# Kernel tuning notes

Measured on AMD Instinct MI355X. Metric: run time of the kernel, lower is better.

## Reference

```python
import jax, jax.numpy as jnp
import numpy as np

N, E, D_IN, D_AGG, D_OUT = 40000, 640000, 128, 128, 64


def setup_inputs() -> dict:
    key = jax.random.key(0)
    ks = jax.random.split(key, 16)

    def lin(kw, fan_in, fan_out):
        s = 1.0 / np.sqrt(fan_in)
        return jax.random.uniform(kw, (fan_in, fan_out), jnp.float32, -s, s)

    return {
        "x_self": jax.random.normal(ks[0], (N, D_IN), jnp.float32),
        "x_neighbor": jax.random.normal(ks[1], (N, D_AGG), jnp.float32),
        "edge_index": jax.random.randint(ks[2], (2, E), 0, N, jnp.int64),
        # linear_in_self: D_IN -> 2*D_OUT
        "W_in_self": lin(ks[3], D_IN, 2 * D_OUT),
        "b_in_self": jnp.zeros((2 * D_OUT,), jnp.float32),
        # linear_out_self: D_IN + 2*D_OUT -> D_OUT
        "W_out_self": lin(ks[4], D_IN + 2 * D_OUT, D_OUT),
        "b_out_self": jnp.zeros((D_OUT,), jnp.float32),
        # gcn1: D_IN -> 2*D_OUT ; gcn2: 2*D_OUT -> D_OUT
        "Wg1": lin(ks[5], D_IN, 2 * D_OUT),
        "bg1": jnp.zeros((2 * D_OUT,), jnp.float32),
        "Wg2": lin(ks[6], 2 * D_OUT, D_OUT),
        "bg2": jnp.zeros((D_OUT,), jnp.float32),
        # linear_out: D_AGG + D_OUT -> D_OUT
        "W_out": lin(ks[7], D_AGG + D_OUT, D_OUT),
        "b_out": jnp.zeros((D_OUT,), jnp.float32),
    }


def _gcn(x, W, b, row, col, norm, n):
    # PyG GCNConv: linear transform, then normalized gather/scatter-add
    h = x @ W                              # [N, out]
    msg = h[row] * norm[:, None]           # [E+N, out] gathered messages
    return jax.ops.segment_sum(msg, col, num_segments=n) + b


def reference(x_self, x_neighbor, edge_index,
              W_in_self, b_in_self, W_out_self, b_out_self,
              Wg1, bg1, Wg2, bg2, W_out, b_out):
    n = x_self.shape[0]
    loop = jnp.arange(n, dtype=edge_index.dtype)
    row = jnp.concatenate([edge_index[0], loop])   # sources (+ self-loops)
    col = jnp.concatenate([edge_index[1], loop])   # targets (+ self-loops)
    deg = jax.ops.segment_sum(jnp.ones_like(col, jnp.float32), col, num_segments=n)
    dis = jnp.where(deg > 0, jax.lax.rsqrt(jnp.maximum(deg, 1.0)), 0.0)
    norm = dis[row] * dis[col]

    # self branch
    l1 = jax.nn.relu(x_self @ W_in_self + b_in_self)
    l1 = jnp.concatenate([x_self, l1], axis=1)
    l1 = l1 @ W_out_self + b_out_self

    # GCN aggregation branch (no activation between convs, per source)
    g1 = _gcn(x_self, Wg1, bg1, row, col, norm, n)
    g2 = _gcn(g1, Wg2, bg2, row, col, norm, n)
    x2 = jnp.concatenate([x_neighbor, g2], axis=1) @ W_out + b_out
    return (l1, x2)
```

## Files before the change

kernel.cpp:

```cpp
#include <hip/hip_runtime.h>

typedef short s8v __attribute__((ext_vector_type(8)));
typedef float f4v __attribute__((ext_vector_type(4)));
typedef unsigned short u16x8 __attribute__((ext_vector_type(8)));

__device__ __forceinline__ unsigned short f2bf(float f) {
  unsigned u = __float_as_uint(f);
  u = (u + 0x7fffu + ((u >> 16) & 1u)) >> 16;
  return (unsigned short)u;
}
__device__ __forceinline__ float bf2f(unsigned short s) {
  return __uint_as_float(((unsigned)s) << 16);
}

#define SLOTS 64

__device__ __forceinline__ void pack_one(const float* __restrict__ W,
                                         unsigned short* __restrict__ P,
                                         int NCf, int stride, int t) {
  const int lane = t & 63;
  const int ct = (t >> 6) % (NCf / 16);
  const int kc = (t >> 6) / (NCf / 16);
  const int col = ct * 16 + (lane & 15);
  const int krow = kc * 32 + (lane >> 4) * 8;
  unsigned short tmp[8];
#pragma unroll
  for (int j = 0; j < 8; ++j) tmp[j] = f2bf(W[(krow + j) * stride + col]);
  uint4 o;
  o.x = (unsigned)tmp[0] | ((unsigned)tmp[1] << 16);
  o.y = (unsigned)tmp[2] | ((unsigned)tmp[3] << 16);
  o.z = (unsigned)tmp[4] | ((unsigned)tmp[5] << 16);
  o.w = (unsigned)tmp[6] | ((unsigned)tmp[7] << 16);
  reinterpret_cast<uint4*>(P)[t] = o;
}

__global__ __launch_bounds__(256) void prep_kernel(
    const float* __restrict__ x, unsigned short* __restrict__ S1,
    int* __restrict__ cnt, const float* __restrict__ Wis,
    const float* __restrict__ Wos, const float* __restrict__ Wo,
    unsigned short* __restrict__ P, int cvtB, int zeroB, int N) {
  const int blk = blockIdx.x;
  const int tid = threadIdx.x;
  if (blk < cvtB) {
    const int i = blk * 256 + tid;
    const float4 v = reinterpret_cast<const float4*>(x)[i];
    ushort4 o;
    o.x = f2bf(v.x); o.y = f2bf(v.y); o.z = f2bf(v.z); o.w = f2bf(v.w);
    reinterpret_cast<ushort4*>(S1)[i] = o;
    return;
  }
  const int b1 = blk - cvtB;
  if (b1 < zeroB) {
    const int i = b1 * 256 + tid;
    if (i < N) cnt[i] = 0;
    return;
  }
  const int b = b1 - zeroB;
  if (b < 4)        pack_one(Wis,            P + 0,     64, 128, b * 256 + tid);
  else if (b < 8)   pack_one(Wis + 64,       P + 8192,  64, 128, (b - 4) * 256 + tid);
  else if (b < 12)  pack_one(Wos,            P + 16384, 64, 64,  (b - 8) * 256 + tid);
  else if (b < 16)  pack_one(Wos + 128 * 64, P + 24576, 64, 64,  (b - 12) * 256 + tid);
  else if (b < 20)  pack_one(Wo,             P + 32768, 64, 64,  (b - 16) * 256 + tid);
  else              pack_one(Wo + 128 * 64,  P + 40960, 64, 64,  (b - 20) * 256 + tid);
}

__device__ __forceinline__ void stage16k(unsigned short* __restrict__ Bs,
                                         const unsigned short* __restrict__ src) {
  uint4* d = reinterpret_cast<uint4*>(Bs);
  const uint4* s = reinterpret_cast<const uint4*>(src);
  for (int i = threadIdx.x; i < 1024; i += 256) d[i] = s[i];
}

__device__ __forceinline__ void load_a_bf16(s8v a[4],
                                            const unsigned short* __restrict__ A,
                                            int arow, int koff) {
#pragma unroll
  for (int kc = 0; kc < 4; ++kc)
    a[kc] = *reinterpret_cast<const s8v*>(A + (long long)arow * 128 + kc * 32 + koff);
}

__device__ __forceinline__ void mfma_panel(f4v acc[4], const s8v a[4],
                                           const unsigned short* __restrict__ Bs,
                                           int lane) {
#pragma unroll
  for (int kc = 0; kc < 4; ++kc)
#pragma unroll
    for (int ct = 0; ct < 4; ++ct) {
      const s8v b =
          *reinterpret_cast<const s8v*>(&Bs[((kc * 4 + ct) * 64 + lane) * 8]);
      acc[ct] = __builtin_amdgcn_mfma_f32_16x16x32_bf16(a[kc], b, acc[ct], 0, 0, 0);
    }
}

__device__ __forceinline__ void gemm1_body(
    unsigned short* __restrict__ Bs, const unsigned short* __restrict__ S1,
    const unsigned short* __restrict__ P, const float* __restrict__ bis,
    unsigned short* __restrict__ S2h, int blk) {
  const int tid = threadIdx.x;
  const int wave = tid >> 6, lane = tid & 63;
  const int row0 = blk * 64 + wave * 16;
  const int arow = row0 + (lane & 15);
  const int koff = (lane >> 4) * 8;
  s8v a1[4];
  load_a_bf16(a1, S1, arow, koff);
  f4v acc[8] = {};
#pragma unroll
  for (int h = 0; h < 2; ++h) {
    if (h) __syncthreads();
    stage16k(Bs, P + h * 8192);
    __syncthreads();
    mfma_panel(&acc[h * 4], a1, Bs, lane);
  }
  const int crow0 = row0 + (lane >> 4) * 4;
  const int ccol = lane & 15;
#pragma unroll
  for (int h = 0; h < 2; ++h)
#pragma unroll
    for (int ctl = 0; ctl < 4; ++ctl) {
      const int col = h * 64 + ctl * 16 + ccol;
      const float bv = bis[col];
#pragma unroll
      for (int r = 0; r < 4; ++r) {
        const float v = fmaxf(acc[h * 4 + ctl][r] + bv, 0.f);
        S2h[(long long)(crow0 + r) * 128 + col] = f2bf(v);
      }
    }
}

__device__ __forceinline__ void gemm2_body(
    unsigned short* __restrict__ Bs, const unsigned short* __restrict__ S1,
    const unsigned short* __restrict__ S2h, const unsigned short* __restrict__ P0,
    const unsigned short* __restrict__ P1, const float* __restrict__ bos,
    float* __restrict__ out1, int blk) {
  const int tid = threadIdx.x;
  const int wave = tid >> 6, lane = tid & 63;
  const int row0 = blk * 64 + wave * 16;
  const int arow = row0 + (lane & 15);
  const int koff = (lane >> 4) * 8;
  s8v a1[4], a2[4];
  load_a_bf16(a1, S1, arow, koff);
  load_a_bf16(a2, S2h, arow, koff);
  f4v acc[4] = {};
  stage16k(Bs, P0);
  __syncthreads();
  mfma_panel(acc, a1, Bs, lane);
  __syncthreads();
  stage16k(Bs, P1);
  __syncthreads();
  mfma_panel(acc, a2, Bs, lane);
  const int crow0 = row0 + (lane >> 4) * 4;
  const int ccol = lane & 15;
#pragma unroll
  for (int ct = 0; ct < 4; ++ct) {
    const int col = ct * 16 + ccol;
    const float bv = bos[col];
#pragma unroll
    for (int r = 0; r < 4; ++r)
      out1[(long long)(crow0 + r) * 64 + col] = acc[ct][r] + bv;
  }
}

template <int K1, bool OUT_BF16, bool A1F32, bool ACCUM>
__device__ __forceinline__ void gemm64_body(
    unsigned short* __restrict__ Bs, const void* __restrict__ A1v,
    const unsigned short* __restrict__ P1, const float* __restrict__ bias,
    void* __restrict__ Cout, int blk) {
  constexpr int KC1 = K1 / 32;
  const int tid = threadIdx.x;
  {
    uint4* d = reinterpret_cast<uint4*>(Bs);
    const uint4* s = reinterpret_cast<const uint4*>(P1);
    constexpr int n1 = K1 * 64 / 8;
    for (int i = tid; i < n1; i += 256) d[i] = s[i];
  }
  const int wave = tid >> 6, lane = tid & 63;
  const int row0 = blk * 64 + wave * 16;
  const int arow = row0 + (lane & 15);
  const int koff = (lane >> 4) * 8;
  s8v a1[KC1];
  if constexpr (A1F32) {
    const float* A1f = (const float*)A1v;
#pragma unroll
    for (int kc = 0; kc < KC1; ++kc) {
      const float4 f0 = *reinterpret_cast<const float4*>(
          A1f + (long long)arow * K1 + kc * 32 + koff);
      const float4 f1 = *reinterpret_cast<const float4*>(
          A1f + (long long)arow * K1 + kc * 32 + koff + 4);
      s8v r;
      r[0] = (short)f2bf(f0.x); r[1] = (short)f2bf(f0.y);
      r[2] = (short)f2bf(f0.z); r[3] = (short)f2bf(f0.w);
      r[4] = (short)f2bf(f1.x); r[5] = (short)f2bf(f1.y);
      r[6] = (short)f2bf(f1.z); r[7] = (short)f2bf(f1.w);
      a1[kc] = r;
    }
  } else {
    const unsigned short* A1b = (const unsigned short*)A1v;
#pragma unroll
    for (int kc = 0; kc < KC1; ++kc)
      a1[kc] = *reinterpret_cast<const s8v*>(A1b + (long long)arow * K1 +
                                             kc * 32 + koff);
  }
  __syncthreads();
  f4v acc[4] = {};
#pragma unroll
  for (int kc = 0; kc < KC1; ++kc)
#pragma unroll
    for (int ct = 0; ct < 4; ++ct) {
      const s8v b =
          *reinterpret_cast<const s8v*>(&Bs[((kc * 4 + ct) * 64 + lane) * 8]);
      acc[ct] = __builtin_amdgcn_mfma_f32_16x16x32_bf16(a1[kc], b, acc[ct], 0, 0, 0);
    }
  const int crow0 = row0 + (lane >> 4) * 4;
  const int ccol = lane & 15;
#pragma unroll
  for (int ct = 0; ct < 4; ++ct) {
    const int col = ct * 16 + ccol;
    const float bv = bias ? bias[col] : 0.f;
#pragma unroll
    for (int r = 0; r < 4; ++r) {
      const long long idx = (long long)(crow0 + r) * 64 + col;
      float v = acc[ct][r] + bv;
      if (ACCUM) v += ((float*)Cout)[idx];
      if (OUT_BF16)
        ((unsigned short*)Cout)[idx] = f2bf(v);
      else
        ((float*)Cout)[idx] = v;
    }
  }
}

template <bool PASS_B>
__device__ __forceinline__ void gather_body(
    const unsigned short* __restrict__ h, const int* __restrict__ csrS,
    const int* __restrict__ cnt, const float* __restrict__ dis,
    float* __restrict__ s_out, const float* __restrict__ s_in,
    const float* __restrict__ bvec, const float* __restrict__ bias,
    unsigned short* __restrict__ out, int N, int gb, int nblk) {
  const int wid = (gb * 256 + (int)threadIdx.x) >> 6;
  const int lane = threadIdx.x & 63;
  const int grp = lane >> 3;
  const int sl = lane & 7;
  const int stride = nblk * 32;

  float bb[8], bv[8];
  if constexpr (PASS_B) {
    const float4 b0 = *reinterpret_cast<const float4*>(bias + sl * 8);
    const float4 b1 = *reinterpret_cast<const float4*>(bias + sl * 8 + 4);
    bb[0] = b0.x; bb[1] = b0.y; bb[2] = b0.z; bb[3] = b0.w;
    bb[4] = b1.x; bb[5] = b1.y; bb[6] = b1.z; bb[7] = b1.w;
    const float4 v0 = *reinterpret_cast<const float4*>(bvec + sl * 8);
    const float4 v1 = *reinterpret_cast<const float4*>(bvec + sl * 8 + 4);
    bv[0] = v0.x; bv[1] = v0.y; bv[2] = v0.z; bv[3] = v0.w;
    bv[4] = v1.x; bv[5] = v1.y; bv[6] = v1.z; bv[7] = v1.w;
  }

  for (int n = wid * 8 + grp; n < N; n += stride) {
    const float dn = dis[n];
    const float dn2 = dn * dn;
    float a[8];
    {
      const u16x8 hv =
          *reinterpret_cast<const u16x8*>(h + (long long)n * 64 + sl * 8);
#pragma unroll
      for (int q = 0; q < 8; ++q) a[q] = bf2f(hv[q]) * dn2;
    }
    float sw = dn2;
    const int deg = min(cnt[n], SLOTS);
    const int* base = csrS + (long long)n * SLOTS;
    int j = 0;
    for (; j + 3 < deg; j += 4) {
      const int4 e = *reinterpret_cast<const int4*>(base + j);
      const u16x8 u0 =
          *reinterpret_cast<const u16x8*>(h + (long long)e.x * 64 + sl * 8);
      const u16x8 u1 =
          *reinterpret_cast<const u16x8*>(h + (long long)e.y * 64 + sl * 8);
      const u16x8 u2 =
          *reinterpret_cast<const u16x8*>(h + (long long)e.z * 64 + sl * 8);
      const u16x8 u3 =
          *reinterpret_cast<const u16x8*>(h + (long long)e.w * 64 + sl * 8);
      const float w0 = dis[e.x] * dn, w1 = dis[e.y] * dn;
      const float w2 = dis[e.z] * dn, w3 = dis[e.w] * dn;
#pragma unroll
      for (int q = 0; q < 8; ++q) {
        a[q] = fmaf(bf2f(u0[q]), w0, a[q]);
        a[q] = fmaf(bf2f(u1[q]), w1, a[q]);
        a[q] = fmaf(bf2f(u2[q]), w2, a[q]);
        a[q] = fmaf(bf2f(u3[q]), w3, a[q]);
      }
      if constexpr (!PASS_B) sw += (w0 + w1) + (w2 + w3);
    }
    for (; j < deg; ++j) {
      const int r = base[j];
      const u16x8 u =
          *reinterpret_cast<const u16x8*>(h + (long long)r * 64 + sl * 8);
      const float w = dis[r] * dn;
#pragma unroll
      for (int q = 0; q < 8; ++q) a[q] = fmaf(bf2f(u[q]), w, a[q]);
      if constexpr (!PASS_B) sw += w;
    }
    u16x8 o;
    if constexpr (!PASS_B) {
      if (sl == 0) s_out[n] = sw;
#pragma unroll
      for (int q = 0; q < 8; ++q) o[q] = f2bf(a[q]);
    } else {
      const float si = s_in[n];
#pragma unroll
      for (int q = 0; q < 8; ++q) o[q] = f2bf(fmaf(si, bv[q], a[q] + bb[q]));
    }
    *reinterpret_cast<u16x8*>(out + (long long)n * 64 + sl * 8) = o;
  }
}

__global__ __launch_bounds__(256) void mega_kernel(
    const unsigned short* __restrict__ S1, const float* __restrict__ x_nb,
    const unsigned short* __restrict__ P, unsigned short* __restrict__ P12,
    const float* __restrict__ bis, const float* __restrict__ bo,
    const float* __restrict__ Wg1, const float* __restrict__ Wg2,
    const float* __restrict__ bg1, float* __restrict__ bvec,
    unsigned short* __restrict__ S2h, unsigned short* __restrict__ S4,
    float* __restrict__ out2, const int* __restrict__ rows,
    const int* __restrict__ cols, int* __restrict__ cnt,
    int* __restrict__ csrS, int E, int degB, int GB) {
  __shared__ unsigned short Bs[8192];
  const int b = blockIdx.x;
  if (b < degB) {
    const int i = b * 256 + (int)threadIdx.x;
    if (i < E) {
      const int c = cols[i];
      const int pos = atomicAdd(&cnt[c], 1);
      if (pos < SLOTS) csrS[(long long)c * SLOTS + pos] = rows[i];
    }
  } else if (b < degB + 33) {
    const int w = b - degB;
    if (w < 32) {
      const int t = w * 256 + (int)threadIdx.x;
      const int i = t >> 6, j = t & 63;
      float acc = 0.f;
      for (int k = 0; k < 128; ++k)
        acc = fmaf(Wg1[i * 128 + k], Wg2[k * 64 + j], acc);
      const int kc = i >> 5;
      const int lane = ((i >> 3) & 3) * 16 + (j & 15);
      const int jj = i & 7;
      const int ct = j >> 4;
      P12[((kc * 4 + ct) * 64 + lane) * 8 + jj] = f2bf(acc);
    } else if (threadIdx.x < 64) {
      const int j = threadIdx.x;
      float acc = 0.f;
      for (int k = 0; k < 128; ++k) acc = fmaf(bg1[k], Wg2[k * 64 + j], acc);
      bvec[j] = acc;
    }
  } else if (b < degB + 33 + GB) {
    gemm64_body<128, false, true, false>(Bs, x_nb, P + 32768, bo, out2,
                                         b - degB - 33);
  } else if (b < degB + 33 + 2 * GB) {
    gemm1_body(Bs, S1, P, bis, S2h, b - degB - 33 - GB);
  } else {
    gemm64_body<128, true, false, false>(Bs, S1, P + 45056, nullptr, S4,
                                         b - degB - 33 - 2 * GB);
  }
}

__global__ __launch_bounds__(256) void dis_kernel(const int* __restrict__ cnt,
                                                  float* __restrict__ dis,
                                                  int N) {
  const int i = blockIdx.x * 256 + threadIdx.x;
  if (i < N) dis[i] = rsqrtf((float)cnt[i] + 1.0f);
}

__global__ __launch_bounds__(256) void g2ga_kernel(
    const unsigned short* __restrict__ S1, const unsigned short* __restrict__ S2h,
    const unsigned short* __restrict__ P, const float* __restrict__ bos,
    float* __restrict__ out1, const unsigned short* __restrict__ S4,
    const int* __restrict__ csrS, const int* __restrict__ cnt,
    const float* __restrict__ dis, float* __restrict__ s_out,
    unsigned short* __restrict__ S3, int N, int GB, int GGB) {
  __shared__ unsigned short Bs[8192];
  const int b = blockIdx.x;
  if (b < GGB) {
    gather_body<false>(S4, csrS, cnt, dis, s_out, nullptr, nullptr, nullptr,
                       S3, N, b, GGB);
  } else {
    gemm2_body(Bs, S1, S2h, P + 16384, P + 24576, bos, out1, b - GGB);
  }
}

__global__ __launch_bounds__(256) void gatherB_kernel(
    const unsigned short* __restrict__ S3, const int* __restrict__ csrS,
    const int* __restrict__ cnt, const float* __restrict__ dis,
    const float* __restrict__ s_in, const float* __restrict__ bvec,
    const float* __restrict__ bias, unsigned short* __restrict__ G2, int N) {
  gather_body<true>(S3, csrS, cnt, dis, nullptr, s_in, bvec, bias, G2, N,
                    blockIdx.x, gridDim.x);
}

__global__ __launch_bounds__(256) void g4b_kernel(
    const unsigned short* __restrict__ G2, const unsigned short* __restrict__ P,
    float* __restrict__ out2) {
  __shared__ unsigned short Bs[4096];
  gemm64_body<64, false, false, true>(Bs, G2, P + 40960, nullptr, out2,
                                      blockIdx.x);
}

extern "C" void kernel_launch(void* const* d_in, const int* in_sizes, int n_in,
                              void* d_out, int out_size, void* d_ws,
                              size_t ws_size, hipStream_t stream) {
  const float* x_self = (const float*)d_in[0];
  const float* x_nb = (const float*)d_in[1];
  const int* ei = (const int*)d_in[2];
  const float* Wis = (const float*)d_in[3];
  const float* bis = (const float*)d_in[4];
  const float* Wos = (const float*)d_in[5];
  const float* bos = (const float*)d_in[6];
  const float* Wg1 = (const float*)d_in[7];
  const float* bg1 = (const float*)d_in[8];
  const float* Wg2 = (const float*)d_in[9];
  const float* bg2 = (const float*)d_in[10];
  const float* Wo = (const float*)d_in[11];
  const float* bo = (const float*)d_in[12];

  const int N = in_sizes[0] / 128;
  const int E = (int)(in_sizes[2] / 2);
  const int* rows = ei;
  const int* cols = ei + E;

  float* out1 = (float*)d_out;
  float* out2 = out1 + (long long)N * 64;

  float* dis = (float*)d_ws;
  int* cnt = (int*)(dis + N);
  float* s = (float*)(cnt + N);
  float* bvec = s + N;
  int* csrS = (int*)(bvec + 64);
  unsigned short* S1 = (unsigned short*)(csrS + (long long)N * SLOTS);
  unsigned short* S2h = S1 + (long long)N * 128;
  unsigned short* S3 = S2h + (long long)N * 128;
  unsigned short* S4 = S3 + (long long)N * 64;
  unsigned short* P = S4 + (long long)N * 64;
  unsigned short* pW12 = P + 45056;

  const int GB = N / 64;
  const int GGB = (N + 31) / 32;

  const int cvtB = (N * 32 + 255) / 256;
  const int zeroB = (N + 255) / 256;
  const int degB = (E + 255) / 256;

  prep_kernel<<<cvtB + zeroB + 22, 256, 0, stream>>>(
      x_self, S1, cnt, Wis, Wos, Wo, P, cvtB, zeroB, N);
  mega_kernel<<<degB + 33 + 3 * GB, 256, 0, stream>>>(
      S1, x_nb, P, pW12, bis, bo, Wg1, Wg2, bg1, bvec, S2h, S4, out2, rows,
      cols, cnt, csrS, E, degB, GB);
  dis_kernel<<<zeroB, 256, 0, stream>>>(cnt, dis, N);
  g2ga_kernel<<<GGB + GB, 256, 0, stream>>>(S1, S2h, P, bos, out1, S4, csrS,
                                            cnt, dis, s, S3, N, GB, GGB);
  gatherB_kernel<<<GGB, 256, 0, stream>>>(S3, csrS, cnt, dis, s, bvec, bg2, S1, N);
  g4b_kernel<<<GB, 256, 0, stream>>>(S1, P, out2);
}
```

Baseline: 115.1 us.

## Drop bf16 pre-conversion and dis kernel; fuse conversion into GEMM loads

Removes the separate fp32-to-bf16 conversion of x_self and has the GEMMs load fp32 directly and convert in registers. The dis kernel is eliminated by recomputing rsqrt(cnt+1) inline in the gathers. The Wg1*Wg2 product and the bias fold move into the prep kernel, and the CSR fill now reads four edges per thread. This cuts one launch and a write/read pass over a bf16 copy of x_self. In exchange the fp32 GEMM loads are twice as wide, the gathers do an extra rsqrt per neighbour, and E is assumed divisible by 4.

After: 105.0 us. 1.1x faster.

```diff
diff --git a/kernel.cpp b/kernel.cpp
--- a/kernel.cpp
+++ b/kernel.cpp
@@ -34,34 +34,42 @@
   reinterpret_cast<uint4*>(P)[t] = o;
 }
 
-__global__ __launch_bounds__(256) void prep_kernel(
-    const float* __restrict__ x, unsigned short* __restrict__ S1,
+__global__ __launch_bounds__(256) void prepA_kernel(
     int* __restrict__ cnt, const float* __restrict__ Wis,
     const float* __restrict__ Wos, const float* __restrict__ Wo,
-    unsigned short* __restrict__ P, int cvtB, int zeroB, int N) {
+    const float* __restrict__ Wg1, const float* __restrict__ Wg2,
+    const float* __restrict__ bg1, unsigned short* __restrict__ P,
+    float* __restrict__ bvec, int zeroB, int N) {
   const int blk = blockIdx.x;
   const int tid = threadIdx.x;
-  if (blk < cvtB) {
+  if (blk < zeroB) {
     const int i = blk * 256 + tid;
-    const float4 v = reinterpret_cast<const float4*>(x)[i];
-    ushort4 o;
-    o.x = f2bf(v.x); o.y = f2bf(v.y); o.z = f2bf(v.z); o.w = f2bf(v.w);
-    reinterpret_cast<ushort4*>(S1)[i] = o;
-    return;
-  }
-  const int b1 = blk - cvtB;
-  if (b1 < zeroB) {
-    const int i = b1 * 256 + tid;
     if (i < N) cnt[i] = 0;
     return;
   }
-  const int b = b1 - zeroB;
+  const int b = blk - zeroB;
   if (b < 4)        pack_one(Wis,            P + 0,     64, 128, b * 256 + tid);
   else if (b < 8)   pack_one(Wis + 64,       P + 8192,  64, 128, (b - 4) * 256 + tid);
   else if (b < 12)  pack_one(Wos,            P + 16384, 64, 64,  (b - 8) * 256 + tid);
   else if (b < 16)  pack_one(Wos + 128 * 64, P + 24576, 64, 64,  (b - 12) * 256 + tid);
   else if (b < 20)  pack_one(Wo,             P + 32768, 64, 64,  (b - 16) * 256 + tid);
-  else              pack_one(Wo + 128 * 64,  P + 40960, 64, 64,  (b - 20) * 256 + tid);
+  else if (b < 22)  pack_one(Wo + 128 * 64,  P + 40960, 64, 64,  (b - 20) * 256 + tid);
+  else if (b < 54) {
+    const int t = (b - 22) * 256 + tid;
+    const int i = t >> 6, j = t & 63;
+    float acc = 0.f;
+    for (int k = 0; k < 128; ++k)
+      acc = fmaf(Wg1[i * 128 + k], Wg2[k * 64 + j], acc);
+    const int kc = i >> 5;
+    const int lane = ((i >> 3) & 3) * 16 + (j & 15);
+    const int jj = i & 7;
+    const int ct = j >> 4;
+    (P + 45056)[((kc * 4 + ct) * 64 + lane) * 8 + jj] = f2bf(acc);
+  } else if (tid < 64) {
+    float acc = 0.f;
+    for (int k = 0; k < 128; ++k) acc = fmaf(bg1[k], Wg2[k * 64 + tid], acc);
+    bvec[tid] = acc;
+  }
 }
 
 __device__ __forceinline__ void stage16k(unsigned short* __restrict__ Bs,
@@ -79,6 +87,24 @@
     a[kc] = *reinterpret_cast<const s8v*>(A + (long long)arow * 128 + kc * 32 + koff);
 }
 
+__device__ __forceinline__ void load_a_f32(s8v a[4],
+                                           const float* __restrict__ A,
+                                           int arow, int koff) {
+#pragma unroll
+  for (int kc = 0; kc < 4; ++kc) {
+    const float4 f0 = *reinterpret_cast<const float4*>(
+        A + (long long)arow * 128 + kc * 32 + koff);
+    const float4 f1 = *reinterpret_cast<const float4*>(
+        A + (long long)arow * 128 + kc * 32 + koff + 4);
+    s8v r;
+    r[0] = (short)f2bf(f0.x); r[1] = (short)f2bf(f0.y);
+    r[2] = (short)f2bf(f0.z); r[3] = (short)f2bf(f0.w);
+    r[4] = (short)f2bf(f1.x); r[5] = (short)f2bf(f1.y);
+    r[6] = (short)f2bf(f1.z); r[7] = (short)f2bf(f1.w);
+    a[kc] = r;
+  }
+}
+
 __device__ __forceinline__ void mfma_panel(f4v acc[4], const s8v a[4],
                                            const unsigned short* __restrict__ Bs,
                                            int lane) {
@@ -93,7 +119,7 @@
 }
 
 __device__ __forceinline__ void gemm1_body(
-    unsigned short* __restrict__ Bs, const unsigned short* __restrict__ S1,
+    unsigned short* __restrict__ Bs, const float* __restrict__ x,
     const unsigned short* __restrict__ P, const float* __restrict__ bis,
     unsigned short* __restrict__ S2h, int blk) {
   const int tid = threadIdx.x;
@@ -102,7 +128,7 @@
   const int arow = row0 + (lane & 15);
   const int koff = (lane >> 4) * 8;
   s8v a1[4];
-  load_a_bf16(a1, S1, arow, koff);
+  load_a_f32(a1, x, arow, koff);
   f4v acc[8] = {};
 #pragma unroll
   for (int h = 0; h < 2; ++h) {
@@ -128,7 +154,7 @@
 }
 
 __device__ __forceinline__ void gemm2_body(
-    unsigned short* __restrict__ Bs, const unsigned short* __restrict__ S1,
+    unsigned short* __restrict__ Bs, const float* __restrict__ x,
     const unsigned short* __restrict__ S2h, const unsigned short* __restrict__ P0,
     const unsigned short* __restrict__ P1, const float* __restrict__ bos,
     float* __restrict__ out1, int blk) {
@@ -138,7 +164,7 @@
   const int arow = row0 + (lane & 15);
   const int koff = (lane >> 4) * 8;
   s8v a1[4], a2[4];
-  load_a_bf16(a1, S1, arow, koff);
+  load_a_f32(a1, x, arow, koff);
   load_a_bf16(a2, S2h, arow, koff);
   f4v acc[4] = {};
   stage16k(Bs, P0);
@@ -232,10 +258,10 @@
 template <bool PASS_B>
 __device__ __forceinline__ void gather_body(
     const unsigned short* __restrict__ h, const int* __restrict__ csrS,
-    const int* __restrict__ cnt, const float* __restrict__ dis,
-    float* __restrict__ s_out, const float* __restrict__ s_in,
-    const float* __restrict__ bvec, const float* __restrict__ bias,
-    unsigned short* __restrict__ out, int N, int gb, int nblk) {
+    const int* __restrict__ cnt, float* __restrict__ s_out,
+    const float* __restrict__ s_in, const float* __restrict__ bvec,
+    const float* __restrict__ bias, unsigned short* __restrict__ out, int N,
+    int gb, int nblk) {
   const int wid = (gb * 256 + (int)threadIdx.x) >> 6;
   const int lane = threadIdx.x & 63;
   const int grp = lane >> 3;
@@ -255,7 +281,8 @@
   }
 
   for (int n = wid * 8 + grp; n < N; n += stride) {
-    const float dn = dis[n];
+    const int cn = cnt[n];
+    const float dn = rsqrtf((float)cn + 1.0f);
     const float dn2 = dn * dn;
     float a[8];
     {
@@ -265,7 +292,7 @@
       for (int q = 0; q < 8; ++q) a[q] = bf2f(hv[q]) * dn2;
     }
     float sw = dn2;
-    const int deg = min(cnt[n], SLOTS);
+    const int deg = min(cn, SLOTS);
     const int* base = csrS + (long long)n * SLOTS;
     int j = 0;
     for (; j + 3 < deg; j += 4) {
@@ -278,8 +305,10 @@
           *reinterpret_cast<const u16x8*>(h + (long long)e.z * 64 + sl * 8);
       const u16x8 u3 =
           *reinterpret_cast<const u16x8*>(h + (long long)e.w * 64 + sl * 8);
-      const float w0 = dis[e.x] * dn, w1 = dis[e.y] * dn;
-      const float w2 = dis[e.z] * dn, w3 = dis[e.w] * dn;
+      const float w0 = rsqrtf((float)cnt[e.x] + 1.0f) * dn;
+      const float w1 = rsqrtf((float)cnt[e.y] + 1.0f) * dn;
+      const float w2 = rsqrtf((float)cnt[e.z] + 1.0f) * dn;
+      const float w3 = rsqrtf((float)cnt[e.w] + 1.0f) * dn;
 #pragma unroll
       for (int q = 0; q < 8; ++q) {
         a[q] = fmaf(bf2f(u0[q]), w0, a[q]);
@@ -293,7 +322,7 @@
       const int r = base[j];
       const u16x8 u =
           *reinterpret_cast<const u16x8*>(h + (long long)r * 64 + sl * 8);
-      const float w = dis[r] * dn;
+      const float w = rsqrtf((float)cnt[r] + 1.0f) * dn;
 #pragma unroll
       for (int q = 0; q < 8; ++q) a[q] = fmaf(bf2f(u[q]), w, a[q]);
       if constexpr (!PASS_B) sw += w;
@@ -313,84 +342,61 @@
 }
 
 __global__ __launch_bounds__(256) void mega_kernel(
-    const unsigned short* __restrict__ S1, const float* __restrict__ x_nb,
-    const unsigned short* __restrict__ P, unsigned short* __restrict__ P12,
-    const float* __restrict__ bis, const float* __restrict__ bo,
-    const float* __restrict__ Wg1, const float* __restrict__ Wg2,
-    const float* __restrict__ bg1, float* __restrict__ bvec,
-    unsigned short* __restrict__ S2h, unsigned short* __restrict__ S4,
-    float* __restrict__ out2, const int* __restrict__ rows,
-    const int* __restrict__ cols, int* __restrict__ cnt,
-    int* __restrict__ csrS, int E, int degB, int GB) {
+    const float* __restrict__ x_self, const float* __restrict__ x_nb,
+    const unsigned short* __restrict__ P, const float* __restrict__ bis,
+    const float* __restrict__ bo, unsigned short* __restrict__ S2h,
+    unsigned short* __restrict__ S4, float* __restrict__ out2,
+    const int* __restrict__ rows, const int* __restrict__ cols,
+    int* __restrict__ cnt, int* __restrict__ csrS, int E4, int fillB, int GB) {
   __shared__ unsigned short Bs[8192];
   const int b = blockIdx.x;
-  if (b < degB) {
-    const int i = b * 256 + (int)threadIdx.x;
-    if (i < E) {
-      const int c = cols[i];
-      const int pos = atomicAdd(&cnt[c], 1);
-      if (pos < SLOTS) csrS[(long long)c * SLOTS + pos] = rows[i];
-    }
-  } else if (b < degB + 33) {
-    const int w = b - degB;
-    if (w < 32) {
-      const int t = w * 256 + (int)threadIdx.x;
-      const int i = t >> 6, j = t & 63;
-      float acc = 0.f;
-      for (int k = 0; k < 128; ++k)
-        acc = fmaf(Wg1[i * 128 + k], Wg2[k * 64 + j], acc);
-      const int kc = i >> 5;
-      const int lane = ((i >> 3) & 3) * 16 + (j & 15);
-      const int jj = i & 7;
-      const int ct = j >> 4;
-      P12[((kc * 4 + ct) * 64 + lane) * 8 + jj] = f2bf(acc);
-    } else if (threadIdx.x < 64) {
-      const int j = threadIdx.x;
-      float acc = 0.f;
-      for (int k = 0; k < 128; ++k) acc = fmaf(bg1[k], Wg2[k * 64 + j], acc);
-      bvec[j] = acc;
-    }
-  } else if (b < degB + 33 + GB) {
+  if (b < fillB) {
+    const int idx = b * 256 + (int)threadIdx.x;
+    if (idx < E4) {
+      const int4 c4 = reinterpret_cast<const int4*>(cols)[idx];
+      const int4 r4 = reinterpret_cast<const int4*>(rows)[idx];
+#pragma unroll
+      for (int k = 0; k < 4; ++k) {
+        const int c = (k == 0) ? c4.x : (k == 1) ? c4.y : (k == 2) ? c4.z : c4.w;
+        const int r = (k == 0) ? r4.x : (k == 1) ? r4.y : (k == 2) ? r4.z : r4.w;
+        const int pos = atomicAdd(&cnt[c], 1);
+        if (pos < SLOTS) csrS[(long long)c * SLOTS + pos] = r;
+      }
+    }
+  } else if (b < fillB + GB) {
+    gemm1_body(Bs, x_self, P, bis, S2h, b - fillB);
+  } else if (b < fillB + 2 * GB) {
+    gemm64_body<128, true, true, false>(Bs, x_self, P + 45056, nullptr, S4,
+                                        b - fillB - GB);
+  } else {
     gemm64_body<128, false, true, false>(Bs, x_nb, P + 32768, bo, out2,
-                                         b - degB - 33);
-  } else if (b < degB + 33 + 2 * GB) {
-    gemm1_body(Bs, S1, P, bis, S2h, b - degB - 33 - GB);
-  } else {
-    gemm64_body<128, true, false, false>(Bs, S1, P + 45056, nullptr, S4,
-                                         b - degB - 33 - 2 * GB);
-  }
-}
-
-__global__ __launch_bounds__(256) void dis_kernel(const int* __restrict__ cnt,
-                                                  float* __restrict__ dis,
-                                                  int N) {
-  const int i = blockIdx.x * 256 + threadIdx.x;
-  if (i < N) dis[i] = rsqrtf((float)cnt[i] + 1.0f);
+                                         b - fillB - 2 * GB);
+  }
 }
 
 __global__ __launch_bounds__(256) void g2ga_kernel(
-    const unsigned short* __restrict__ S1, const unsigned short* __restrict__ S2h,
+    const float* __restrict__ x_self, const unsigned short* __restrict__ S2h,
     const unsigned short* __restrict__ P, const float* __restrict__ bos,
     float* __restrict__ out1, const unsigned short* __restrict__ S4,
     const int* __restrict__ csrS, const int* __restrict__ cnt,
-    const float* __restrict__ dis, float* __restrict__ s_out,
-    unsigned short* __restrict__ S3, int N, int GB, int GGB) {
+    float* __restrict__ s_out, unsigned short* __restrict__ S3, int N, int GB,
+    int GGB) {
   __shared__ unsigned short Bs[8192];
   const int b = blockIdx.x;
   if (b < GGB) {
-    gather_body<false>(S4, csrS, cnt, dis, s_out, nullptr, nullptr, nullptr,
-                       S3, N, b, GGB);
+    gather_body<false>(S4, csrS, cnt, s_out, nullptr, nullptr, nullptr, S3, N,
+                       b, GGB);
   } else {
-    gemm2_body(Bs, S1, S2h, P + 16384, P + 24576, bos, out1, b - GGB);
+    gemm2_body(Bs, x_self, S2h, P + 16384, P + 24576, bos, out1, b - GGB);
   }
 }
 
 __global__ __launch_bounds__(256) void gatherB_kernel(
     const unsigned short* __restrict__ S3, const int* __restrict__ csrS,
-    const int* __restrict__ cnt, const float* __restrict__ dis,
-    const float* __restrict__ s_in, const float* __restrict__ bvec,
-    const float* __restrict__ bias, unsigned short* __restrict__ G2, int N) {
-  gather_body<true>(S3, csrS, cnt, dis, nullptr, s_in, bvec, bias, G2, N,
+    const int* __restrict__ cnt, const float* __restrict__ s_in,
+    const float* __restrict__ bvec, const float* __restrict__ bias,
+    unsigned short* __restrict__ G2, int N) {
+  gather_body<true>(S3, csrS, cnt, nullptr, s_in, bvec, bias, G2, N,
                     blockIdx.x, gridDim.x);
 }
 
@@ -427,33 +433,31 @@
   float* out1 = (float*)d_out;
   float* out2 = out1 + (long long)N * 64;
 
-  float* dis = (float*)d_ws;
-  int* cnt = (int*)(dis + N);
+  int* cnt = (int*)d_ws;
   float* s = (float*)(cnt + N);
   float* bvec = s + N;
   int* csrS = (int*)(bvec + 64);
-  unsigned short* S1 = (unsigned short*)(csrS + (long long)N * SLOTS);
-  unsigned short* S2h = S1 + (long long)N * 128;
+  unsigned short* S2h = (unsigned short*)(csrS + (long long)N * SLOTS);
   unsigned short* S3 = S2h + (long long)N * 128;
   unsigned short* S4 = S3 + (long long)N * 64;
-  unsigned short* P = S4 + (long long)N * 64;
+  unsigned short* G2 = S4 + (long long)N * 64;
+  unsigned short* P = G2 + (long long)N * 64;
   unsigned short* pW12 = P + 45056;
 
   const int GB = N / 64;
   const int GGB = (N + 31) / 32;
 
-  const int cvtB = (N * 32 + 255) / 256;
   const int zeroB = (N + 255) / 256;
-  const int degB = (E + 255) / 256;
-
-  prep_kernel<<<cvtB + zeroB + 22, 256, 0, stream>>>(
-      x_self, S1, cnt, Wis, Wos, Wo, P, cvtB, zeroB, N);
-  mega_kernel<<<degB + 33 + 3 * GB, 256, 0, stream>>>(
-      S1, x_nb, P, pW12, bis, bo, Wg1, Wg2, bg1, bvec, S2h, S4, out2, rows,
-      cols, cnt, csrS, E, degB, GB);
-  dis_kernel<<<zeroB, 256, 0, stream>>>(cnt, dis, N);
-  g2ga_kernel<<<GGB + GB, 256, 0, stream>>>(S1, S2h, P, bos, out1, S4, csrS,
-                                            cnt, dis, s, S3, N, GB, GGB);
-  gatherB_kernel<<<GGB, 256, 0, stream>>>(S3, csrS, cnt, dis, s, bvec, bg2, S1, N);
-  g4b_kernel<<<GB, 256, 0, stream>>>(S1, P, out2);
-}
+  const int E4 = E / 4;
+  const int fillB = (E4 + 255) / 256;
+
+  prepA_kernel<<<zeroB + 55, 256, 0, stream>>>(cnt, Wis, Wos, Wo, Wg1, Wg2,
+                                               bg1, P, bvec, zeroB, N);
+  mega_kernel<<<fillB + 3 * GB, 256, 0, stream>>>(
+      x_self, x_nb, P, bis, bo, S2h, S4, out2, rows, cols, cnt, csrS, E4,
+      fillB, GB);
+  g2ga_kernel<<<GGB + GB, 256, 0, stream>>>(x_self, S2h, P, bos, out1, S4,
+                                            csrS, cnt, s, S3, N, GB, GGB);
+  gatherB_kernel<<<GGB, 256, 0, stream>>>(S3, csrS, cnt, s, bvec, bg2, G2, N);
+  g4b_kernel<<<GB, 256, 0, stream>>>(G2, P, out2);
+}
```
